# Kernel tuning notes

Measured on AMD Instinct MI355X. Metric: run time of the kernel, lower is better.

Reference implementation:

```python
import jax, jax.numpy as jnp
import numpy as np
from jax import lax

NEG = -1e30  # finite stand-in for -inf (avoids NaN grads)
EPS = 1e-7   # keras backend epsilon used by ctc_batch_cost: log(y_pred + eps)

B, T, C, L = 64, 2048, 128, 256


def setup_inputs() -> dict:
    key = jax.random.key(0)
    k1, k2 = jax.random.split(key)
    # labels in [0, C-2]; blank index is C-1 per keras ctc_batch_cost convention
    y_true = jax.random.randint(k1, (B, L), 0, C - 1, dtype=jnp.int32).astype(jnp.int64)
    # y_pred are (unnormalized) per-frame class probabilities, as keras expects softmax output
    y_pred = jax.random.uniform(k2, (B, T, C), dtype=jnp.float32)
    return {"y_true": y_true, "y_pred": y_pred}


def _lse3(a, b, c):
    s = jnp.stack([a, b, c], axis=0)
    m = jnp.max(s, axis=0)
    return m + jnp.log(jnp.sum(jnp.exp(s - m), axis=0))


def _ctc_loss(y_true, y_pred):
    """Faithful jnp version of K.ctc_batch_cost with full input/label lengths."""
    b, t, c = y_pred.shape
    l = y_true.shape[1]
    blank = c - 1
    S = 2 * l + 1

    logp = jnp.log(y_pred + EPS)  # [B,T,C]

    labels = y_true.astype(jnp.int32)
    # extended label sequence: blank, l1, blank, l2, ..., blank  -> [B,S]
    ext = jnp.full((b, S), blank, dtype=jnp.int32).at[:, 1::2].set(labels)
    # gather per-frame log-probs of extended labels -> [B,T,S]
    lp_z = jnp.take_along_axis(logp, jnp.broadcast_to(ext[:, None, :], (b, t, S)), axis=2)

    # skip transition allowed at s if z[s] != blank and z[s] != z[s-2]
    ext_m2 = jnp.concatenate([jnp.full((b, 2), blank, jnp.int32), ext[:, :-2]], axis=1)
    skip = (ext != blank) & (ext != ext_m2) & (jnp.arange(S)[None, :] >= 2)  # [B,S]

    lp_tbs = jnp.transpose(lp_z, (1, 0, 2))  # [T,B,S]

    neg = jnp.full((b, S), NEG, dtype=logp.dtype)
    alpha0 = neg.at[:, 0].set(lp_tbs[0][:, 0]).at[:, 1].set(lp_tbs[0][:, 1])

    neg1 = jnp.full((b, 1), NEG, dtype=logp.dtype)
    neg2 = jnp.full((b, 2), NEG, dtype=logp.dtype)

    def step(alpha, lp_t):
        s1 = jnp.concatenate([neg1, alpha[:, :-1]], axis=1)
        s2 = jnp.where(skip, jnp.concatenate([neg2, alpha[:, :-2]], axis=1), NEG)
        new = _lse3(alpha, s1, s2) + lp_t
        return new, None

    alphaT, _ = lax.scan(step, alpha0, lp_tbs[1:])
    loss = -jnp.logaddexp(alphaT[:, -1], alphaT[:, -2])  # [B]
    return loss[:, None]  # keras ctc_batch_cost returns [B,1]


def reference(y_true, y_pred):
    return _ctc_loss(y_true, y_pred)
```

## Files before the change

kernel.cpp:

```cpp
#include <hip/hip_runtime.h>


#define B_ 64
#define T_ 2048
#define C_ 128
#define L_ 256
#define BLANK_ (C_ - 1)
#define EPSF 1e-7f
#define LN2F 0.69314718055994530942f
#define CH_ 16
#define SENT_ (-(1 << 28))

typedef __attribute__((address_space(1))) const void glob_cv;
typedef __attribute__((address_space(3))) void lds_v;
typedef __attribute__((address_space(3))) float lds_f;

__device__ __forceinline__ void gl2lds16(const void* g, void* l) {
    __builtin_amdgcn_global_load_lds((glob_cv*)g, (lds_v*)l, 16, 0, 0);
}

#define WAIT_VM(n) asm volatile("s_waitcnt vmcnt(" #n ")" ::: "memory")
#define WAIT_LGKM(n) do { \
    asm volatile("s_waitcnt lgkmcnt(" #n ")" ::: "memory"); \
    __builtin_amdgcn_sched_barrier(0); } while (0)
#define DSR(dst, p, off) \
    asm volatile("ds_read_b32 %0, %1 offset:%2" : "=v"(dst) : "v"(p), "i"(off))

__device__ __forceinline__ float dpp_shr1_f(float x) {
    return __int_as_float(
        __builtin_amdgcn_update_dpp(0, __float_as_int(x), 0x138, 0xf, 0xf, false));
}
__device__ __forceinline__ int dpp_shr1_i(int x) {
    return __builtin_amdgcn_update_dpp(0, x, 0x138, 0xf, 0xf, false);
}
__device__ __forceinline__ float dpp_shl1_f(float x) {
    return __int_as_float(
        __builtin_amdgcn_update_dpp(0, __float_as_int(x), 0x130, 0xf, 0xf, false));
}
__device__ __forceinline__ int dpp_shl1_i(int x) {
    return __builtin_amdgcn_update_dpp(0, x, 0x130, 0xf, 0xf, false);
}

struct G { float pb, p1, p3, p5, p7; };

__launch_bounds__(128, 1)
__global__ void ctc_loss_kernel(const int* __restrict__ y_true,
                                const float* __restrict__ y_pred,
                                float* __restrict__ out) {
    const int b = blockIdx.x;
    const int tid = threadIdx.x;
    const int w = __builtin_amdgcn_readfirstlane(tid >> 6);
    const int l = tid & 63;

    __shared__ float ring[2][4][CH_ * C_];

    const int* __restrict__ lab = y_true + b * L_;
    const int4 lv = *(const int4*)(lab + 4 * l);
    const int e1 = lv.x, e3 = lv.y, e5 = lv.z, e7 = lv.w;
    const int em1 = (l > 0) ? lab[4 * l - 1] : -1;
    const float m1f = ((l > 0) && (e1 != em1)) ? 1.0f : 0.0f;
    const float m3f = (e3 != e1) ? 1.0f : 0.0f;
    const float m5f = (e5 != e3) ? 1.0f : 0.0f;
    const float m7f = (e7 != e5) ? 1.0f : 0.0f;
    const float m8f = (l == 63) ? 1.0f : 0.0f;

    const float* __restrict__ base = y_pred + (size_t)b * (T_ * C_);

    lds_f* const lbase = (lds_f*)&ring[0][0][0];
    const int relem = w * 8192;
    lds_f* const pB = lbase + relem + BLANK_;
    lds_f* const p1p = lbase + relem + e1;
    lds_f* const p3p = lbase + relem + e3;
    lds_f* const p5p = lbase + relem + e5;
    lds_f* const p7p = lbase + relem + e7;

    G g[4];
    auto fill = [&](int slot, int off) {
        DSR(g[slot].pb, pB, off);
        DSR(g[slot].p1, p1p, off);
        DSR(g[slot].p3, p3p, off);
        DSR(g[slot].p5, p5p, off);
        DSR(g[slot].p7, p7p, off);
    };

    auto issue_chunk = [&](int t0, int buf) {
        const float* gp = base + (size_t)t0 * C_ + 4 * l;
        float* d = &ring[w][buf][0];
#pragma unroll
        for (int i = 0; i < 8; ++i)
            gl2lds16(gp + i * 256, d + i * 256);
    };

    float a0 = 0.f, a1 = 0.f, a2 = 0.f, a3 = 0.f, a4 = 0.f,
          a5 = 0.f, a6 = 0.f, a7 = 0.f, a8 = 0.f;
    int E = SENT_;
    float upscale = 1.0f;

    auto step = [&](const G& q) {
        const float pb = q.pb + EPSF, p1 = q.p1 + EPSF, p3 = q.p3 + EPSF,
                    p5 = q.p5 + EPSF, p7 = q.p7 + EPSF;
        const float up = dpp_shr1_f(a7) * upscale;
        const float n0 = (a0 + up) * pb;
        const float n1 = fmaf(m1f, up, a0 + a1) * p1;
        const float n2 = (a1 + a2) * pb;
        const float n3 = fmaf(m3f, a1, a2 + a3) * p3;
        const float n4 = (a3 + a4) * pb;
        const float n5 = fmaf(m5f, a3, a4 + a5) * p5;
        const float n6 = (a5 + a6) * pb;
        const float n7 = fmaf(m7f, a5, a6 + a7) * p7;
        const float n8 = fmaf(m8f, a7, a8) * pb;
        a0 = n0; a1 = n1; a2 = n2; a3 = n3; a4 = n4;
        a5 = n5; a6 = n6; a7 = n7; a8 = n8;
    };

    auto boundary = [&]() {
        float mx = fmaxf(fmaxf(fmaxf(a0, a1), fmaxf(a2, a3)),
                         fmaxf(fmaxf(a4, a5), fmaxf(a6, a7)));
        mx = fmaxf(mx, a8);
        const bool z = (mx == 0.0f);
        const int e = (int)(__float_as_uint(mx) >> 23) - 127;
        const float s = z ? 1.0f : __uint_as_float((unsigned)(127 - e) << 23);
        a0 *= s; a1 *= s; a2 *= s; a3 *= s; a4 *= s;
        a5 *= s; a6 *= s; a7 *= s; a8 *= s;
        E = z ? SENT_ : (E + e);
        int upE = dpp_shr1_i(E);
        if (l == 0) upE = SENT_;
        if (E == SENT_) E = upE;
        int d = upE - E;
        d = min(max(d, -126), 120);
        upscale = __uint_as_float((unsigned)(d + 127) << 23);
    };

    auto run_chunk = [&](int bc, int bn, int jstart, bool last) {
#pragma unroll
        for (int j = 0; j < CH_; ++j) {
            if (j == 0 && jstart) continue;
            if (!last || j <= 12) { WAIT_LGKM(15); }
            else if (j == 13)     { WAIT_LGKM(10); }
            else if (j == 14)     { WAIT_LGKM(5); }
            else                  { WAIT_LGKM(0); }
            step(g[j & 3]);
            if (!last || j < 12) {
                const int off = (j < 12) ? (bc * 8192 + (j + 4) * 512)
                                         : (bn * 8192 + (j - 12) * 512);
                fill(j & 3, off);
            }
            if ((j & 3) == 3) boundary();
        }
    };

    auto stepb = [&](const G& q) {
        const float pb = q.pb + EPSF, p1 = q.p1 + EPSF, p3 = q.p3 + EPSF,
                    p5 = q.p5 + EPSF, p7 = q.p7 + EPSF;
        const float d0 = a0 * pb, d1 = a1 * p1, d2 = a2 * pb,
                    d3 = a3 * p3, d4 = a4 * pb, d5 = a5 * p5,
                    d6 = a6 * pb, d7 = a7 * p7, d8 = a8 * pb;
        const float u = fmaf(m1f, d1, d0);
        const float dn = dpp_shl1_f(u) * upscale;
        a0 = d0 + d1;
        a1 = fmaf(m3f, d3, d1 + d2);
        a2 = d2 + d3;
        a3 = fmaf(m5f, d5, d3 + d4);
        a4 = d4 + d5;
        a5 = fmaf(m7f, d7, d5 + d6);
        a6 = d6 + d7;
        a7 = fmaf(m8f, d8, d7 + dn);
        a8 = d8;
    };

    auto boundaryb = [&]() {
        float mx = fmaxf(fmaxf(fmaxf(a0, a1), fmaxf(a2, a3)),
                         fmaxf(fmaxf(a4, a5), fmaxf(a6, a7)));
        mx = fmaxf(mx, a8);
        const bool z = (mx == 0.0f);
        const int e = (int)(__float_as_uint(mx) >> 23) - 127;
        const float s = z ? 1.0f : __uint_as_float((unsigned)(127 - e) << 23);
        a0 *= s; a1 *= s; a2 *= s; a3 *= s; a4 *= s;
        a5 *= s; a6 *= s; a7 *= s; a8 *= s;
        E = z ? SENT_ : (E + e);
        int upE = dpp_shl1_i(E);
        if (l == 63) upE = SENT_;
        if (E == SENT_) E = upE;
        int d = upE - E;
        d = min(max(d, -126), 120);
        upscale = __uint_as_float((unsigned)(d + 127) << 23);
    };

    auto run_chunkb = [&](int bc, int bn, bool last) {
#pragma unroll
        for (int j = 0; j < CH_; ++j) {
            if (!last || j <= 12) { WAIT_LGKM(15); }
            else if (j == 13)     { WAIT_LGKM(10); }
            else if (j == 14)     { WAIT_LGKM(5); }
            else                  { WAIT_LGKM(0); }
            stepb(g[j & 3]);
            if (!last || j < 12) {
                const int off = (j < 12) ? (bc * 8192 + (11 - j) * 512)
                                         : (bn * 8192 + (27 - j) * 512);
                fill(j & 3, off);
            }
            if ((j & 3) == 3) boundaryb();
        }
    };

    if (w == 0) {
        issue_chunk(0, 0);
        issue_chunk(CH_, 1);
        issue_chunk(2 * CH_, 2);

        WAIT_VM(8);
        issue_chunk(3 * CH_, 3);
        {
            const float* rbf = &ring[0][0][0];
            if (l == 0) { a0 = rbf[BLANK_] + EPSF; a1 = rbf[e1] + EPSF; E = 0; }
        }
        boundary();
        fill(1, 1 * 512);
        fill(2, 2 * 512);
        fill(3, 3 * 512);
        fill(0, 4 * 512);
        run_chunk(0, 1, 1, false);
        WAIT_VM(8); issue_chunk(4 * CH_, 0); run_chunk(1, 2, 0, false);
        WAIT_VM(8); issue_chunk(5 * CH_, 1); run_chunk(2, 3, 0, false);
        WAIT_VM(8); issue_chunk(6 * CH_, 2); run_chunk(3, 0, 0, false);

#pragma unroll 1
        for (int m = 1; m <= 14; ++m) {
            const int c = 4 * m;
            WAIT_VM(8); issue_chunk((c + 3) * CH_, 3); run_chunk(0, 1, 0, false);
            WAIT_VM(8); issue_chunk((c + 4) * CH_, 0); run_chunk(1, 2, 0, false);
            WAIT_VM(8); issue_chunk((c + 5) * CH_, 1); run_chunk(2, 3, 0, false);
            WAIT_VM(8); issue_chunk((c + 6) * CH_, 2); run_chunk(3, 0, 0, false);
        }

        WAIT_VM(8); issue_chunk(63 * CH_, 3); run_chunk(0, 1, 0, false);
        WAIT_VM(8);
        run_chunk(1, 2, 0, false);
        WAIT_VM(0);
        run_chunk(2, 3, 0, false);
        run_chunk(3, 3, 0, true);
    } else {
        auto issq = [&](int q, int buf) { issue_chunk((127 - q) * CH_, buf); };
        issq(0, 0); issq(1, 1); issq(2, 2);

        WAIT_VM(8);
        issq(3, 3);
        if (l == 63) { a7 = 1.0f; a8 = 1.0f; E = 0; }
        boundaryb();
        fill(0, 15 * 512); fill(1, 14 * 512); fill(2, 13 * 512); fill(3, 12 * 512);
        run_chunkb(0, 1, false);
        WAIT_VM(8); issq(4, 0); run_chunkb(1, 2, false);
        WAIT_VM(8); issq(5, 1); run_chunkb(2, 3, false);
        WAIT_VM(8); issq(6, 2); run_chunkb(3, 0, false);

#pragma unroll 1
        for (int m = 1; m <= 14; ++m) {
            const int c = 4 * m;
            WAIT_VM(8); issq(c + 3, 3); run_chunkb(0, 1, false);
            WAIT_VM(8); issq(c + 4, 0); run_chunkb(1, 2, false);
            WAIT_VM(8); issq(c + 5, 1); run_chunkb(2, 3, false);
            WAIT_VM(8); issq(c + 6, 2); run_chunkb(3, 0, false);
        }

        WAIT_VM(8); issq(63, 3); run_chunkb(0, 1, false);
        WAIT_VM(8);
        run_chunkb(1, 2, false);
        WAIT_VM(0);
        run_chunkb(2, 3, false);
        run_chunkb(3, 3, true);
        float* xf = &ring[1][0][0];
        xf[0 * 64 + l] = a0; xf[1 * 64 + l] = a1; xf[2 * 64 + l] = a2;
        xf[3 * 64 + l] = a3; xf[4 * 64 + l] = a4; xf[5 * 64 + l] = a5;
        xf[6 * 64 + l] = a6; xf[7 * 64 + l] = a7; xf[8 * 64 + l] = a8;
        ((int*)xf)[9 * 64 + l] = E;
    }

    __syncthreads();

    if (w == 0) {
        const float* xf = &ring[1][0][0];
        float sd = a0 * xf[0 * 64 + l];
        sd = fmaf(a1, xf[1 * 64 + l], sd);
        sd = fmaf(a2, xf[2 * 64 + l], sd);
        sd = fmaf(a3, xf[3 * 64 + l], sd);
        sd = fmaf(a4, xf[4 * 64 + l], sd);
        sd = fmaf(a5, xf[5 * 64 + l], sd);
        sd = fmaf(a6, xf[6 * 64 + l], sd);
        sd = fmaf(a7, xf[7 * 64 + l], sd);
        sd = fmaf(a8, xf[8 * 64 + l], sd);
        const int E2 = ((const int*)xf)[9 * 64 + l];
        const bool nz = (sd > 0.0f);
        int Es = nz ? (E + E2) : SENT_;
        int M = Es;
#pragma unroll
        for (int o = 32; o; o >>= 1) M = max(M, __shfl_xor(M, o));
        int d = Es - M;
        d = max(d, -126);
        float val = nz ? sd * __uint_as_float((unsigned)(d + 127) << 23) : 0.0f;
#pragma unroll
        for (int o = 32; o; o >>= 1) val += __shfl_xor(val, o);
        if (l == 0) out[b] = -(__logf(val) + (float)M * LN2F);
    }
}

extern "C" void kernel_launch(void* const* d_in, const int* in_sizes, int n_in,
                              void* d_out, int out_size, void* d_ws, size_t ws_size,
                              hipStream_t stream) {
    const int* y_true = (const int*)d_in[0];
    const float* y_pred = (const float*)d_in[1];
    float* out = (float*)d_out;
    ctc_loss_kernel<<<B_, 128, 0, stream>>>(y_true, y_pred, out);
}
```

Baseline: 179.8 us.

## Replace LDS ring staging with direct per-lane global gathers in register ring

Drops the global-to-LDS async chunk ring (with its manual vmcnt/lgkmcnt waits and ds_read gathers) and has each lane load its five needed class probabilities per frame straight from global memory into an 8-deep register prefetch ring. This removes full-row LDS staging traffic and the hand-scheduled wait logic, and cuts shared memory to a small transfer buffer. In exchange each step now depends on scattered global loads, which rely on cache hits and hardware latency hiding rather than explicit bulk prefetch, and only 8 frames of lookahead.

```diff
diff --git a/kernel.cpp b/kernel.cpp
--- a/kernel.cpp
+++ b/kernel.cpp
@@ -8,23 +8,7 @@
 #define BLANK_ (C_ - 1)
 #define EPSF 1e-7f
 #define LN2F 0.69314718055994530942f
-#define CH_ 16
 #define SENT_ (-(1 << 28))
-
-typedef __attribute__((address_space(1))) const void glob_cv;
-typedef __attribute__((address_space(3))) void lds_v;
-typedef __attribute__((address_space(3))) float lds_f;
-
-__device__ __forceinline__ void gl2lds16(const void* g, void* l) {
-    __builtin_amdgcn_global_load_lds((glob_cv*)g, (lds_v*)l, 16, 0, 0);
-}
-
-#define WAIT_VM(n) asm volatile("s_waitcnt vmcnt(" #n ")" ::: "memory")
-#define WAIT_LGKM(n) do { \
-    asm volatile("s_waitcnt lgkmcnt(" #n ")" ::: "memory"); \
-    __builtin_amdgcn_sched_barrier(0); } while (0)
-#define DSR(dst, p, off) \
-    asm volatile("ds_read_b32 %0, %1 offset:%2" : "=v"(dst) : "v"(p), "i"(off))
 
 __device__ __forceinline__ float dpp_shr1_f(float x) {
     return __int_as_float(
@@ -52,7 +36,7 @@
     const int w = __builtin_amdgcn_readfirstlane(tid >> 6);
     const int l = tid & 63;
 
-    __shared__ float ring[2][4][CH_ * C_];
+    __shared__ float xfer[640];
 
     const int* __restrict__ lab = y_true + b * L_;
     const int4 lv = *(const int4*)(lab + 4 * l);
@@ -66,30 +50,21 @@
 
     const float* __restrict__ base = y_pred + (size_t)b * (T_ * C_);
 
-    lds_f* const lbase = (lds_f*)&ring[0][0][0];
-    const int relem = w * 8192;
-    lds_f* const pB = lbase + relem + BLANK_;
-    lds_f* const p1p = lbase + relem + e1;
-    lds_f* const p3p = lbase + relem + e3;
-    lds_f* const p5p = lbase + relem + e5;
-    lds_f* const p7p = lbase + relem + e7;
-
-    G g[4];
-    auto fill = [&](int slot, int off) {
-        DSR(g[slot].pb, pB, off);
-        DSR(g[slot].p1, p1p, off);
-        DSR(g[slot].p3, p3p, off);
-        DSR(g[slot].p5, p5p, off);
-        DSR(g[slot].p7, p7p, off);
-    };
-
-    auto issue_chunk = [&](int t0, int buf) {
-        const float* gp = base + (size_t)t0 * C_ + 4 * l;
-        float* d = &ring[w][buf][0];
-#pragma unroll
-        for (int i = 0; i < 8; ++i)
-            gl2lds16(gp + i * 256, d + i * 256);
-    };
+    const float* pB;
+    const float* q1;
+    const float* q3;
+    const float* q5;
+    const float* q7;
+
+    G g[8];
+    auto fill = [&](int s, int off) {
+        g[s].pb = pB[off];
+        g[s].p1 = q1[off];
+        g[s].p3 = q3[off];
+        g[s].p5 = q5[off];
+        g[s].p7 = q7[off];
+    };
+    auto adv = [&](int d) { pB += d; q1 += d; q3 += d; q5 += d; q7 += d; };
 
     float a0 = 0.f, a1 = 0.f, a2 = 0.f, a3 = 0.f, a4 = 0.f,
           a5 = 0.f, a6 = 0.f, a7 = 0.f, a8 = 0.f;
@@ -129,24 +104,6 @@
         int d = upE - E;
         d = min(max(d, -126), 120);
         upscale = __uint_as_float((unsigned)(d + 127) << 23);
-    };
-
-    auto run_chunk = [&](int bc, int bn, int jstart, bool last) {
-#pragma unroll
-        for (int j = 0; j < CH_; ++j) {
-            if (j == 0 && jstart) continue;
-            if (!last || j <= 12) { WAIT_LGKM(15); }
-            else if (j == 13)     { WAIT_LGKM(10); }
-            else if (j == 14)     { WAIT_LGKM(5); }
-            else                  { WAIT_LGKM(0); }
-            step(g[j & 3]);
-            if (!last || j < 12) {
-                const int off = (j < 12) ? (bc * 8192 + (j + 4) * 512)
-                                         : (bn * 8192 + (j - 12) * 512);
-                fill(j & 3, off);
-            }
-            if ((j & 3) == 3) boundary();
-        }
     };
 
     auto stepb = [&](const G& q) {
@@ -186,109 +143,75 @@
         upscale = __uint_as_float((unsigned)(d + 127) << 23);
     };
 
-    auto run_chunkb = [&](int bc, int bn, bool last) {
-#pragma unroll
-        for (int j = 0; j < CH_; ++j) {
-            if (!last || j <= 12) { WAIT_LGKM(15); }
-            else if (j == 13)     { WAIT_LGKM(10); }
-            else if (j == 14)     { WAIT_LGKM(5); }
-            else                  { WAIT_LGKM(0); }
-            stepb(g[j & 3]);
-            if (!last || j < 12) {
-                const int off = (j < 12) ? (bc * 8192 + (11 - j) * 512)
-                                         : (bn * 8192 + (27 - j) * 512);
-                fill(j & 3, off);
+    if (w == 0) {
+        pB = base + BLANK_; q1 = base + e1; q3 = base + e3;
+        q5 = base + e5; q7 = base + e7;
+#pragma unroll
+        for (int s = 0; s < 8; ++s) fill(s, s * C_);
+        if (l == 0) { a0 = g[0].pb + EPSF; a1 = g[0].p1 + EPSF; E = 0; }
+        boundary();
+        adv(8 * C_);
+        fill(0, 0);
+#pragma unroll
+        for (int s = 1; s < 8; ++s) {
+            step(g[s]); fill(s, s * C_);
+            if ((s & 3) == 3) boundary();
+        }
+#pragma unroll 1
+        for (int m = 1; m <= 126; ++m) {
+            adv(8 * C_);
+#pragma unroll
+            for (int s = 0; s < 8; ++s) {
+                step(g[s]); fill(s, s * C_);
+                if ((s & 3) == 3) boundary();
             }
-            if ((j & 3) == 3) boundaryb();
-        }
-    };
-
-    if (w == 0) {
-        issue_chunk(0, 0);
-        issue_chunk(CH_, 1);
-        issue_chunk(2 * CH_, 2);
-
-        WAIT_VM(8);
-        issue_chunk(3 * CH_, 3);
-        {
-            const float* rbf = &ring[0][0][0];
-            if (l == 0) { a0 = rbf[BLANK_] + EPSF; a1 = rbf[e1] + EPSF; E = 0; }
-        }
-        boundary();
-        fill(1, 1 * 512);
-        fill(2, 2 * 512);
-        fill(3, 3 * 512);
-        fill(0, 4 * 512);
-        run_chunk(0, 1, 1, false);
-        WAIT_VM(8); issue_chunk(4 * CH_, 0); run_chunk(1, 2, 0, false);
-        WAIT_VM(8); issue_chunk(5 * CH_, 1); run_chunk(2, 3, 0, false);
-        WAIT_VM(8); issue_chunk(6 * CH_, 2); run_chunk(3, 0, 0, false);
-
-#pragma unroll 1
-        for (int m = 1; m <= 14; ++m) {
-            const int c = 4 * m;
-            WAIT_VM(8); issue_chunk((c + 3) * CH_, 3); run_chunk(0, 1, 0, false);
-            WAIT_VM(8); issue_chunk((c + 4) * CH_, 0); run_chunk(1, 2, 0, false);
-            WAIT_VM(8); issue_chunk((c + 5) * CH_, 1); run_chunk(2, 3, 0, false);
-            WAIT_VM(8); issue_chunk((c + 6) * CH_, 2); run_chunk(3, 0, 0, false);
-        }
-
-        WAIT_VM(8); issue_chunk(63 * CH_, 3); run_chunk(0, 1, 0, false);
-        WAIT_VM(8);
-        run_chunk(1, 2, 0, false);
-        WAIT_VM(0);
-        run_chunk(2, 3, 0, false);
-        run_chunk(3, 3, 0, true);
+        }
+#pragma unroll
+        for (int s = 0; s < 8; ++s) {
+            step(g[s]);
+            if ((s & 3) == 3) boundary();
+        }
     } else {
-        auto issq = [&](int q, int buf) { issue_chunk((127 - q) * CH_, buf); };
-        issq(0, 0); issq(1, 1); issq(2, 2);
-
-        WAIT_VM(8);
-        issq(3, 3);
+        const float* bb = base + 2047 * C_;
+        pB = bb + BLANK_; q1 = bb + e1; q3 = bb + e3;
+        q5 = bb + e5; q7 = bb + e7;
+#pragma unroll
+        for (int s = 0; s < 8; ++s) fill(s, -(s * C_));
         if (l == 63) { a7 = 1.0f; a8 = 1.0f; E = 0; }
         boundaryb();
-        fill(0, 15 * 512); fill(1, 14 * 512); fill(2, 13 * 512); fill(3, 12 * 512);
-        run_chunkb(0, 1, false);
-        WAIT_VM(8); issq(4, 0); run_chunkb(1, 2, false);
-        WAIT_VM(8); issq(5, 1); run_chunkb(2, 3, false);
-        WAIT_VM(8); issq(6, 2); run_chunkb(3, 0, false);
-
 #pragma unroll 1
-        for (int m = 1; m <= 14; ++m) {
-            const int c = 4 * m;
-            WAIT_VM(8); issq(c + 3, 3); run_chunkb(0, 1, false);
-            WAIT_VM(8); issq(c + 4, 0); run_chunkb(1, 2, false);
-            WAIT_VM(8); issq(c + 5, 1); run_chunkb(2, 3, false);
-            WAIT_VM(8); issq(c + 6, 2); run_chunkb(3, 0, false);
-        }
-
-        WAIT_VM(8); issq(63, 3); run_chunkb(0, 1, false);
-        WAIT_VM(8);
-        run_chunkb(1, 2, false);
-        WAIT_VM(0);
-        run_chunkb(2, 3, false);
-        run_chunkb(3, 3, true);
-        float* xf = &ring[1][0][0];
-        xf[0 * 64 + l] = a0; xf[1 * 64 + l] = a1; xf[2 * 64 + l] = a2;
-        xf[3 * 64 + l] = a3; xf[4 * 64 + l] = a4; xf[5 * 64 + l] = a5;
-        xf[6 * 64 + l] = a6; xf[7 * 64 + l] = a7; xf[8 * 64 + l] = a8;
-        ((int*)xf)[9 * 64 + l] = E;
+        for (int m = 0; m <= 126; ++m) {
+            adv(-8 * C_);
+#pragma unroll
+            for (int s = 0; s < 8; ++s) {
+                stepb(g[s]); fill(s, -(s * C_));
+                if ((s & 3) == 3) boundaryb();
+            }
+        }
+#pragma unroll
+        for (int s = 0; s < 8; ++s) {
+            stepb(g[s]);
+            if ((s & 3) == 3) boundaryb();
+        }
+        xfer[0 * 64 + l] = a0; xfer[1 * 64 + l] = a1; xfer[2 * 64 + l] = a2;
+        xfer[3 * 64 + l] = a3; xfer[4 * 64 + l] = a4; xfer[5 * 64 + l] = a5;
+        xfer[6 * 64 + l] = a6; xfer[7 * 64 + l] = a7; xfer[8 * 64 + l] = a8;
+        ((int*)xfer)[9 * 64 + l] = E;
     }
 
     __syncthreads();
 
     if (w == 0) {
-        const float* xf = &ring[1][0][0];
-        float sd = a0 * xf[0 * 64 + l];
-        sd = fmaf(a1, xf[1 * 64 + l], sd);
-        sd = fmaf(a2, xf[2 * 64 + l], sd);
-        sd = fmaf(a3, xf[3 * 64 + l], sd);
-        sd = fmaf(a4, xf[4 * 64 + l], sd);
-        sd = fmaf(a5, xf[5 * 64 + l], sd);
-        sd = fmaf(a6, xf[6 * 64 + l], sd);
-        sd = fmaf(a7, xf[7 * 64 + l], sd);
-        sd = fmaf(a8, xf[8 * 64 + l], sd);
-        const int E2 = ((const int*)xf)[9 * 64 + l];
+        float sd = a0 * xfer[0 * 64 + l];
+        sd = fmaf(a1, xfer[1 * 64 + l], sd);
+        sd = fmaf(a2, xfer[2 * 64 + l], sd);
+        sd = fmaf(a3, xfer[3 * 64 + l], sd);
+        sd = fmaf(a4, xfer[4 * 64 + l], sd);
+        sd = fmaf(a5, xfer[5 * 64 + l], sd);
+        sd = fmaf(a6, xfer[6 * 64 + l], sd);
+        sd = fmaf(a7, xfer[7 * 64 + l], sd);
+        sd = fmaf(a8, xfer[8 * 64 + l], sd);
+        const int E2 = ((const int*)xfer)[9 * 64 + l];
         const bool nz = (sd > 0.0f);
         int Es = nz ? (E + E2) : SENT_;
         int M = Es;
```

Result: slower. 211.6 us (+17.7%).
